# Optimization experiments

Measured on AMD Instinct MI355X. Metric: run time of the kernel, lower is better.

## Reference

```python
import jax, jax.numpy as jnp
import numpy as np

C = 128          # in_channels
NODE_NUM = 8192  # number of unique source nodes this step
D = 64           # max_member_num (fixed degree -> neighbor_bool all True)
E = NODE_NUM * D # total gathered neighbor slots
N_TOTAL = 200000 # total nodes in graph
NEG_SLOPE = 0.2


def setup_inputs() -> dict:
    key = jax.random.key(0)
    ks = jax.random.split(key, 8)
    node_features = jax.random.normal(ks[0], (N_TOTAL, C), jnp.float32)
    memory = jax.random.normal(ks[1], (N_TOTAL, C), jnp.float32)
    sc = 1.0 / np.sqrt(C)
    W_max = jax.random.normal(ks[2], (C, C), jnp.float32) * sc
    b_max = jnp.zeros((C,), jnp.float32)
    W_score = jax.random.normal(ks[3], (2 * C, 1), jnp.float32) * (1.0 / np.sqrt(2 * C))
    b_score = jnp.zeros((1,), jnp.float32)
    W_fit = jax.random.normal(ks[4], (C, 1), jnp.float32) * sc
    b_fit = jnp.zeros((1,), jnp.float32)
    neighbors = jax.random.randint(ks[5], (E,), 0, N_TOTAL)  # gathered neighbor node ids
    seg = jnp.repeat(jnp.arange(NODE_NUM), D)                # index_source_nodes (segment ids)
    return dict(node_features=node_features, memory=memory, W_max=W_max, b_max=b_max,
                W_score=W_score, b_score=b_score, W_fit=W_fit, b_fit=b_fit,
                neighbors=neighbors, seg=seg)


def reference(node_features, memory, W_max, b_max, W_score, b_score, W_fit, b_fit, neighbors, seg):
    # gather: features + detached memory per neighbor slot  [E, C]
    nbr = node_features[neighbors] + jax.lax.stop_gradient(memory[neighbors])
    # scatter_max per source node, then linear + re-gather duplication
    max_feature = jax.ops.segment_max(nbr, seg, num_segments=NODE_NUM)      # [node_num, C]
    max_lin = max_feature @ W_max + b_max                                    # [node_num, C]
    dup = max_lin[seg]                                                       # [E, C]
    # attention score over concat(center_max, neighbor)
    s = jnp.concatenate([dup, nbr], axis=-1) @ W_score + b_score             # [E, 1]
    s = jnp.where(s >= 0, s, NEG_SLOPE * s)                                  # leaky_relu
    # segment softmax over neighbors of each source node
    smax = jax.ops.segment_max(s, seg, num_segments=NODE_NUM)[seg]
    ex = jnp.exp(s - smax)
    denom = jax.ops.segment_sum(ex, seg, num_segments=NODE_NUM)[seg]
    score = ex / denom                                                       # [E, 1]
    # masked scatter into fixed [node_num, max_member_num] tensor (full mask -> reshape)
    score_tensor = score.reshape(NODE_NUM, D)
    # scatter_add pooling of score-weighted neighbor features
    cluster_feature = jax.ops.segment_sum(nbr * score, seg, num_segments=NODE_NUM)  # [node_num, C]
    # community fitness via linear score calculator + sigmoid
    fitness = jax.nn.sigmoid(cluster_feature @ W_fit + b_fit).reshape(-1)    # [node_num]
    return cluster_feature, score_tensor, fitness
```

## Files before the change

### kernel.cpp

```cpp
#include <hip/hip_runtime.h>
#include <hip/hip_fp16.h>
#include <math.h>

#define C_DIM 128
#define DEG 64
#define NEG_SLOPE 0.2f

typedef float nfloat4 __attribute__((ext_vector_type(4)));

__global__ __launch_bounds__(256)
void fuse_sum_half_kernel(const nfloat4* __restrict__ nf4,
                          const nfloat4* __restrict__ mem4,
                          float2* __restrict__ outh,
                          long n4,
                          const float* __restrict__ W_max,
                          const float* __restrict__ b_max,
                          const float* __restrict__ W_score,
                          const float* __restrict__ b_score,
                          float* __restrict__ combo) {
    const long base = (long)blockIdx.x * 1024 + threadIdx.x;
    if (base + 768 < n4) {
        nfloat4 a0 = __builtin_nontemporal_load(nf4 + base);
        nfloat4 a1 = __builtin_nontemporal_load(nf4 + base + 256);
        nfloat4 a2 = __builtin_nontemporal_load(nf4 + base + 512);
        nfloat4 a3 = __builtin_nontemporal_load(nf4 + base + 768);
        nfloat4 m0 = __builtin_nontemporal_load(mem4 + base);
        nfloat4 m1 = __builtin_nontemporal_load(mem4 + base + 256);
        nfloat4 m2 = __builtin_nontemporal_load(mem4 + base + 512);
        nfloat4 m3 = __builtin_nontemporal_load(mem4 + base + 768);
        const nfloat4 s0 = a0 + m0, s1 = a1 + m1, s2 = a2 + m2, s3 = a3 + m3;
        __half2 p0[2], p1[2], p2[2], p3[2];
        p0[0] = __floats2half2_rn(s0.x, s0.y); p0[1] = __floats2half2_rn(s0.z, s0.w);
        p1[0] = __floats2half2_rn(s1.x, s1.y); p1[1] = __floats2half2_rn(s1.z, s1.w);
        p2[0] = __floats2half2_rn(s2.x, s2.y); p2[1] = __floats2half2_rn(s2.z, s2.w);
        p3[0] = __floats2half2_rn(s3.x, s3.y); p3[1] = __floats2half2_rn(s3.z, s3.w);
        outh[base]       = *(const float2*)p0;
        outh[base + 256] = *(const float2*)p1;
        outh[base + 512] = *(const float2*)p2;
        outh[base + 768] = *(const float2*)p3;
    } else {
        #pragma unroll
        for (int k = 0; k < 4; ++k) {
            const long i = base + k * 256;
            if (i < n4) {
                const nfloat4 a = __builtin_nontemporal_load(nf4 + i);
                const nfloat4 m = __builtin_nontemporal_load(mem4 + i);
                const nfloat4 s = a + m;
                __half2 p[2];
                p[0] = __floats2half2_rn(s.x, s.y);
                p[1] = __floats2half2_rn(s.z, s.w);
                outh[i] = *(const float2*)p;
            }
        }
    }
    if (blockIdx.x == 0) {
        const int c = threadIdx.x;
        __shared__ float red[C_DIM];
        if (c < C_DIM) {
            float acc = 0.f;
            #pragma unroll 4
            for (int k = 0; k < C_DIM; ++k)
                acc += W_max[c * C_DIM + k] * W_score[k];
            combo[c] = acc;
            red[c] = b_max[c] * W_score[c];
        }
        __syncthreads();
        for (int off = 64; off > 0; off >>= 1) {
            if (c < off) red[c] += red[c + off];
            __syncthreads();
        }
        if (c == 0) combo[C_DIM] = red[0] + b_score[0];
    }
}

__global__ __launch_bounds__(256)
void detector_half2_kernel(const float4* __restrict__ sum4,
                           const float* __restrict__ W_score,
                           const float* __restrict__ W_fit,
                           const float* __restrict__ b_fit,
                           const int* __restrict__ neighbors,
                           const float* __restrict__ combo,
                           float* __restrict__ out_cf,
                           float* __restrict__ out_score,
                           float* __restrict__ out_fit) {
    __shared__ float4 red4[2][256][2];
    __shared__ float  chan[2][C_DIM];
    __shared__ float  s_raw[2][DEG];
    __shared__ float  sc[2][DEG];

    const int tid = threadIdx.x;
    const int n0  = blockIdx.x * 2;
    const int q   = tid & 15;
    const int g   = tid >> 4;

    int4 nb[2];
    nb[0] = ((const int4*)(neighbors + (long)n0 * DEG))[g];
    nb[1] = ((const int4*)(neighbors + (long)(n0 + 1) * DEG))[g];

    const float4 wsb0 = ((const float4*)(W_score + C_DIM))[2 * q];
    const float4 wsb1 = ((const float4*)(W_score + C_DIM))[2 * q + 1];

    float4 vh[2][4];
    {
        const int ids0[4] = {nb[0].x, nb[0].y, nb[0].z, nb[0].w};
        const int ids1[4] = {nb[1].x, nb[1].y, nb[1].z, nb[1].w};
        #pragma unroll
        for (int i = 0; i < 4; ++i) vh[0][i] = sum4[(long)ids0[i] * 16 + q];
        #pragma unroll
        for (int i = 0; i < 4; ++i) vh[1][i] = sum4[(long)ids1[i] * 16 + q];
    }
    asm volatile("" ::: "memory");

    #pragma unroll
    for (int p = 0; p < 2; ++p) {
        float mx[8];
        #pragma unroll
        for (int k = 0; k < 8; ++k) mx[k] = -INFINITY;
        #pragma unroll
        for (int i = 0; i < 4; ++i) {
            const __half2* hp = (const __half2*)&vh[p][i];
            const float2 f0 = __half22float2(hp[0]);
            const float2 f1 = __half22float2(hp[1]);
            const float2 f2 = __half22float2(hp[2]);
            const float2 f3 = __half22float2(hp[3]);
            mx[0] = fmaxf(mx[0], f0.x); mx[1] = fmaxf(mx[1], f0.y);
            mx[2] = fmaxf(mx[2], f1.x); mx[3] = fmaxf(mx[3], f1.y);
            mx[4] = fmaxf(mx[4], f2.x); mx[5] = fmaxf(mx[5], f2.y);
            mx[6] = fmaxf(mx[6], f3.x); mx[7] = fmaxf(mx[7], f3.y);
            float pd = f0.x * wsb0.x + f0.y * wsb0.y + f1.x * wsb0.z + f1.y * wsb0.w
                     + f2.x * wsb1.x + f2.y * wsb1.y + f3.x * wsb1.z + f3.y * wsb1.w;
            pd += __shfl_xor(pd, 1);
            pd += __shfl_xor(pd, 2);
            pd += __shfl_xor(pd, 4);
            pd += __shfl_xor(pd, 8);
            if (q == 0) s_raw[p][g * 4 + i] = pd;
        }
        red4[p][tid][0] = make_float4(mx[0], mx[1], mx[2], mx[3]);
        red4[p][tid][1] = make_float4(mx[4], mx[5], mx[6], mx[7]);
    }
    __syncthreads();

    {
        const int p = tid >> 7, c = tid & 127;
        const int ch = c >> 3, k = c & 7;
        const float* rp = (const float*)red4[p];
        float f = rp[ch * 8 + k];
        #pragma unroll
        for (int g2 = 1; g2 < 16; ++g2)
            f = fmaxf(f, rp[(g2 * 16 + ch) * 8 + k]);
        chan[p][c] = f * combo[c];
    }
    __syncthreads();

    if (tid < 128) {
        const int p = tid >> 6, slot = tid & 63;
        float t1 = chan[p][slot] + chan[p][slot + 64];
        #pragma unroll
        for (int msk = 1; msk <= 32; msk <<= 1)
            t1 += __shfl_xor(t1, msk);
        t1 += combo[C_DIM];
        float s = t1 + s_raw[p][slot];
        s = (s >= 0.f) ? s : NEG_SLOPE * s;
        float m = s;
        #pragma unroll
        for (int msk = 1; msk <= 32; msk <<= 1)
            m = fmaxf(m, __shfl_xor(m, msk));
        const float ex = __expf(s - m);
        float d = ex;
        #pragma unroll
        for (int msk = 1; msk <= 32; msk <<= 1)
            d += __shfl_xor(d, msk);
        const float sv = ex / d;
        sc[p][slot] = sv;
        out_score[(long)(n0 + p) * DEG + slot] = sv;
    }
    __syncthreads();

    #pragma unroll
    for (int p = 0; p < 2; ++p) {
        float acc[8] = {0.f, 0.f, 0.f, 0.f, 0.f, 0.f, 0.f, 0.f};
        #pragma unroll
        for (int i = 0; i < 4; ++i) {
            const float w = sc[p][g * 4 + i];
            const __half2* hp = (const __half2*)&vh[p][i];
            const float2 f0 = __half22float2(hp[0]);
            const float2 f1 = __half22float2(hp[1]);
            const float2 f2 = __half22float2(hp[2]);
            const float2 f3 = __half22float2(hp[3]);
            acc[0] += f0.x * w; acc[1] += f0.y * w;
            acc[2] += f1.x * w; acc[3] += f1.y * w;
            acc[4] += f2.x * w; acc[5] += f2.y * w;
            acc[6] += f3.x * w; acc[7] += f3.y * w;
        }
        red4[p][tid][0] = make_float4(acc[0], acc[1], acc[2], acc[3]);
        red4[p][tid][1] = make_float4(acc[4], acc[5], acc[6], acc[7]);
    }
    __syncthreads();

    {
        const int p = tid >> 7, c = tid & 127;
        const int ch = c >> 3, k = c & 7;
        const float* rp = (const float*)red4[p];
        float f = 0.f;
        #pragma unroll
        for (int g2 = 0; g2 < 16; ++g2)
            f += rp[(g2 * 16 + ch) * 8 + k];
        out_cf[(long)(n0 + p) * C_DIM + c] = f;
        chan[p][c] = f * W_fit[c];
    }
    __syncthreads();

    if (tid < 128) {
        const int p = tid >> 6, slot = tid & 63;
        float t = chan[p][slot] + chan[p][slot + 64];
        #pragma unroll
        for (int msk = 1; msk <= 32; msk <<= 1)
            t += __shfl_xor(t, msk);
        if (slot == 0)
            out_fit[n0 + p] = 1.f / (1.f + __expf(-(t + b_fit[0])));
    }
}

__global__ void precompute_kernel(const float* __restrict__ W_max,
                                  const float* __restrict__ b_max,
                                  const float* __restrict__ W_score,
                                  const float* __restrict__ b_score,
                                  float* __restrict__ combo) {
    const int c = threadIdx.x;
    float acc = 0.f;
    for (int k = 0; k < C_DIM; ++k)
        acc += W_max[c * C_DIM + k] * W_score[k];
    combo[c] = acc;
    __shared__ float red[C_DIM];
    red[c] = b_max[c] * W_score[c];
    __syncthreads();
    for (int off = 64; off > 0; off >>= 1) {
        if (c < off) red[c] += red[c + off];
        __syncthreads();
    }
    if (c == 0) combo[C_DIM] = red[0] + b_score[0];
}

__global__ __launch_bounds__(256)
void detector_f32_kernel(const float* __restrict__ nf,
                         const float* __restrict__ mem,
                         const float* __restrict__ W_score,
                         const float* __restrict__ W_fit,
                         const float* __restrict__ b_fit,
                         const int* __restrict__ neighbors,
                         const float* __restrict__ combo,
                         float* __restrict__ out_cf,
                         float* __restrict__ out_score,
                         float* __restrict__ out_fit) {
    __shared__ float4 red[256];
    __shared__ float  s_raw[DEG];
    __shared__ float  sc[DEG];
    __shared__ float  t1_sh;

    const int tid = threadIdx.x;
    const int n   = blockIdx.x;
    const int q   = tid & 31;
    const int g   = tid >> 5;

    const int4* nb4 = (const int4*)(neighbors + n * DEG + g * 8);
    const int4 nba = nb4[0];
    const int4 nbb = nb4[1];
    const int ids[8] = {nba.x, nba.y, nba.z, nba.w, nbb.x, nbb.y, nbb.z, nbb.w};
    const float4 wsb = ((const float4*)(W_score + C_DIM))[q];
    const float4* nf4  = (const float4*)nf;
    const float4* mem4 = (const float4*)mem;

    float4 v[8];
    float4 mx = make_float4(-INFINITY, -INFINITY, -INFINITY, -INFINITY);
    #pragma unroll
    for (int i = 0; i < 8; ++i) {
        const long node = ids[i];
        float4 vv = nf4[node * 32 + q];
        const float4 b = mem4[node * 32 + q];
        vv.x += b.x; vv.y += b.y; vv.z += b.z; vv.w += b.w;
        v[i] = vv;
        mx.x = fmaxf(mx.x, vv.x); mx.y = fmaxf(mx.y, vv.y);
        mx.z = fmaxf(mx.z, vv.z); mx.w = fmaxf(mx.w, vv.w);
        float p = vv.x * wsb.x + vv.y * wsb.y + vv.z * wsb.z + vv.w * wsb.w;
        p += __shfl_xor(p, 1); p += __shfl_xor(p, 2); p += __shfl_xor(p, 4);
        p += __shfl_xor(p, 8); p += __shfl_xor(p, 16);
        if (q == 0) s_raw[g * 8 + i] = p;
    }
    asm volatile("" ::: "memory");
    red[tid] = mx;
    __syncthreads();
    if (tid < 32) {
        float4 f = red[tid];
        #pragma unroll
        for (int r = 1; r < 8; ++r) {
            const float4 o = red[tid + 32 * r];
            f.x = fmaxf(f.x, o.x); f.y = fmaxf(f.y, o.y);
            f.z = fmaxf(f.z, o.z); f.w = fmaxf(f.w, o.w);
        }
        const float4 wc = ((const float4*)combo)[tid];
        float t1 = f.x * wc.x + f.y * wc.y + f.z * wc.z + f.w * wc.w;
        t1 += __shfl_xor(t1, 1); t1 += __shfl_xor(t1, 2); t1 += __shfl_xor(t1, 4);
        t1 += __shfl_xor(t1, 8); t1 += __shfl_xor(t1, 16);
        if (tid == 0) t1_sh = t1 + combo[C_DIM];
    }
    __syncthreads();
    if (tid < DEG) {
        float s = t1_sh + s_raw[tid];
        s = (s >= 0.f) ? s : NEG_SLOPE * s;
        float m = s;
        #pragma unroll
        for (int msk = 1; msk <= 32; msk <<= 1) m = fmaxf(m, __shfl_xor(m, msk));
        const float ex = __expf(s - m);
        float d = ex;
        #pragma unroll
        for (int msk = 1; msk <= 32; msk <<= 1) d += __shfl_xor(d, msk);
        const float sv = ex / d;
        sc[tid] = sv;
        out_score[n * DEG + tid] = sv;
    }
    __syncthreads();
    float4 acc = make_float4(0.f, 0.f, 0.f, 0.f);
    #pragma unroll
    for (int i = 0; i < 8; ++i) {
        const float w = sc[g * 8 + i];
        acc.x += v[i].x * w; acc.y += v[i].y * w;
        acc.z += v[i].z * w; acc.w += v[i].w * w;
    }
    red[tid] = acc;
    __syncthreads();
    if (tid < 32) {
        float4 f = red[tid];
        #pragma unroll
        for (int r = 1; r < 8; ++r) {
            const float4 o = red[tid + 32 * r];
            f.x += o.x; f.y += o.y; f.z += o.z; f.w += o.w;
        }
        ((float4*)(out_cf + (long)n * C_DIM))[tid] = f;
        const float4 wf = ((const float4*)W_fit)[tid];
        float fp = f.x * wf.x + f.y * wf.y + f.z * wf.z + f.w * wf.w;
        fp += __shfl_xor(fp, 1); fp += __shfl_xor(fp, 2); fp += __shfl_xor(fp, 4);
        fp += __shfl_xor(fp, 8); fp += __shfl_xor(fp, 16);
        if (tid == 0)
            out_fit[n] = 1.f / (1.f + __expf(-(fp + b_fit[0])));
    }
}

extern "C" void kernel_launch(void* const* d_in, const int* in_sizes, int n_in,
                              void* d_out, int out_size, void* d_ws, size_t ws_size,
                              hipStream_t stream) {
    const float* node_features = (const float*)d_in[0];
    const float* memory        = (const float*)d_in[1];
    const float* W_max         = (const float*)d_in[2];
    const float* b_max         = (const float*)d_in[3];
    const float* W_score       = (const float*)d_in[4];
    const float* b_score       = (const float*)d_in[5];
    const float* W_fit         = (const float*)d_in[6];
    const float* b_fit         = (const float*)d_in[7];
    const int*   neighbors     = (const int*)d_in[8];

    const long n_elem = (long)in_sizes[0];
    const int  nodes  = in_sizes[8] / DEG;
    const long n4     = n_elem / 4;

    float* combo = (float*)d_ws;
    __half* sumh = (__half*)(combo + 512);
    const size_t need = 512 * sizeof(float) + (size_t)n_elem * sizeof(__half);

    float* out_cf    = (float*)d_out;
    float* out_score = out_cf + (long)nodes * C_DIM;
    float* out_fit   = out_score + (long)nodes * DEG;

    if (ws_size >= need && (n_elem % 4) == 0 && (nodes % 2) == 0) {
        const int blocks = (int)((n4 + 1023) / 1024);
        fuse_sum_half_kernel<<<blocks, 256, 0, stream>>>(
            (const nfloat4*)node_features, (const nfloat4*)memory,
            (float2*)sumh, n4, W_max, b_max, W_score, b_score, combo);
        detector_half2_kernel<<<nodes / 2, 256, 0, stream>>>(
            (const float4*)sumh, W_score, W_fit, b_fit, neighbors, combo,
            out_cf, out_score, out_fit);
    } else {
        precompute_kernel<<<1, C_DIM, 0, stream>>>(W_max, b_max, W_score,
                                                   b_score, combo);
        detector_f32_kernel<<<nodes, 256, 0, stream>>>(
            node_features, memory, W_score, W_fit, b_fit, neighbors, combo,
            out_cf, out_score, out_fit);
    }
}
```

Measured before the change: 247.2 us.

## Process four nodes per block and use wave shuffles for channel reductions

The detector kernel now handles four source nodes per 256-thread block instead of two, so each thread keeps 16 gathered neighbor vectors in flight. The max and weighted-sum channel reductions first combine across lanes with shuffles, then finish over four waves through a small padded shared buffer instead of a 16-way shared-memory pass. The streaming fp16 pre-sum kernel doubles its per-thread work to eight float4 pairs. The aim is more memory-level parallelism and less shared-memory traffic, at the cost of higher register pressure and fewer blocks in flight.

Measured after the change: 259.5 us. +5.0%, slower.

```diff
diff --git a/kernel.cpp b/kernel.cpp
--- a/kernel.cpp
+++ b/kernel.cpp
@@ -18,29 +18,24 @@
                           const float* __restrict__ W_score,
                           const float* __restrict__ b_score,
                           float* __restrict__ combo) {
-    const long base = (long)blockIdx.x * 1024 + threadIdx.x;
-    if (base + 768 < n4) {
-        nfloat4 a0 = __builtin_nontemporal_load(nf4 + base);
-        nfloat4 a1 = __builtin_nontemporal_load(nf4 + base + 256);
-        nfloat4 a2 = __builtin_nontemporal_load(nf4 + base + 512);
-        nfloat4 a3 = __builtin_nontemporal_load(nf4 + base + 768);
-        nfloat4 m0 = __builtin_nontemporal_load(mem4 + base);
-        nfloat4 m1 = __builtin_nontemporal_load(mem4 + base + 256);
-        nfloat4 m2 = __builtin_nontemporal_load(mem4 + base + 512);
-        nfloat4 m3 = __builtin_nontemporal_load(mem4 + base + 768);
-        const nfloat4 s0 = a0 + m0, s1 = a1 + m1, s2 = a2 + m2, s3 = a3 + m3;
-        __half2 p0[2], p1[2], p2[2], p3[2];
-        p0[0] = __floats2half2_rn(s0.x, s0.y); p0[1] = __floats2half2_rn(s0.z, s0.w);
-        p1[0] = __floats2half2_rn(s1.x, s1.y); p1[1] = __floats2half2_rn(s1.z, s1.w);
-        p2[0] = __floats2half2_rn(s2.x, s2.y); p2[1] = __floats2half2_rn(s2.z, s2.w);
-        p3[0] = __floats2half2_rn(s3.x, s3.y); p3[1] = __floats2half2_rn(s3.z, s3.w);
-        outh[base]       = *(const float2*)p0;
-        outh[base + 256] = *(const float2*)p1;
-        outh[base + 512] = *(const float2*)p2;
-        outh[base + 768] = *(const float2*)p3;
+    const long base = (long)blockIdx.x * 2048 + threadIdx.x;
+    if (base + 1792 < n4) {
+        nfloat4 a[8], m[8];
+        #pragma unroll
+        for (int k = 0; k < 8; ++k) a[k] = __builtin_nontemporal_load(nf4 + base + k * 256);
+        #pragma unroll
+        for (int k = 0; k < 8; ++k) m[k] = __builtin_nontemporal_load(mem4 + base + k * 256);
+        #pragma unroll
+        for (int k = 0; k < 8; ++k) {
+            const nfloat4 s = a[k] + m[k];
+            __half2 p[2];
+            p[0] = __floats2half2_rn(s.x, s.y);
+            p[1] = __floats2half2_rn(s.z, s.w);
+            outh[base + k * 256] = *(const float2*)p;
+        }
     } else {
         #pragma unroll
-        for (int k = 0; k < 4; ++k) {
+        for (int k = 0; k < 8; ++k) {
             const long i = base + k * 256;
             if (i < n4) {
                 const nfloat4 a = __builtin_nontemporal_load(nf4 + i);
@@ -74,7 +69,7 @@
 }
 
 __global__ __launch_bounds__(256)
-void detector_half2_kernel(const float4* __restrict__ sum4,
+void detector_half4_kernel(const float4* __restrict__ sum4,
                            const float* __restrict__ W_score,
                            const float* __restrict__ W_fit,
                            const float* __restrict__ b_fit,
@@ -83,36 +78,37 @@
                            float* __restrict__ out_cf,
                            float* __restrict__ out_score,
                            float* __restrict__ out_fit) {
-    __shared__ float4 red4[2][256][2];
-    __shared__ float  chan[2][C_DIM];
-    __shared__ float  s_raw[2][DEG];
-    __shared__ float  sc[2][DEG];
+    __shared__ float wred[4][4][16][9];
+    __shared__ float chan[4][C_DIM];
+    __shared__ float s_raw[4][DEG];
+    __shared__ float sc[4][DEG];
 
     const int tid = threadIdx.x;
-    const int n0  = blockIdx.x * 2;
+    const int n0  = blockIdx.x * 4;
     const int q   = tid & 15;
     const int g   = tid >> 4;
-
-    int4 nb[2];
-    nb[0] = ((const int4*)(neighbors + (long)n0 * DEG))[g];
-    nb[1] = ((const int4*)(neighbors + (long)(n0 + 1) * DEG))[g];
+    const int wv  = tid >> 6;
+    const int ln  = tid & 63;
+
+    int4 nb[4];
+    #pragma unroll
+    for (int p = 0; p < 4; ++p)
+        nb[p] = ((const int4*)(neighbors + (long)(n0 + p) * DEG))[g];
 
     const float4 wsb0 = ((const float4*)(W_score + C_DIM))[2 * q];
     const float4 wsb1 = ((const float4*)(W_score + C_DIM))[2 * q + 1];
 
-    float4 vh[2][4];
-    {
-        const int ids0[4] = {nb[0].x, nb[0].y, nb[0].z, nb[0].w};
-        const int ids1[4] = {nb[1].x, nb[1].y, nb[1].z, nb[1].w};
-        #pragma unroll
-        for (int i = 0; i < 4; ++i) vh[0][i] = sum4[(long)ids0[i] * 16 + q];
-        #pragma unroll
-        for (int i = 0; i < 4; ++i) vh[1][i] = sum4[(long)ids1[i] * 16 + q];
+    float4 vh[4][4];
+    #pragma unroll
+    for (int p = 0; p < 4; ++p) {
+        const int ids[4] = {nb[p].x, nb[p].y, nb[p].z, nb[p].w};
+        #pragma unroll
+        for (int i = 0; i < 4; ++i) vh[p][i] = sum4[(long)ids[i] * 16 + q];
     }
     asm volatile("" ::: "memory");
 
     #pragma unroll
-    for (int p = 0; p < 2; ++p) {
+    for (int p = 0; p < 4; ++p) {
         float mx[8];
         #pragma unroll
         for (int k = 0; k < 8; ++k) mx[k] = -INFINITY;
@@ -135,25 +131,33 @@
             pd += __shfl_xor(pd, 8);
             if (q == 0) s_raw[p][g * 4 + i] = pd;
         }
-        red4[p][tid][0] = make_float4(mx[0], mx[1], mx[2], mx[3]);
-        red4[p][tid][1] = make_float4(mx[4], mx[5], mx[6], mx[7]);
+        #pragma unroll
+        for (int k = 0; k < 8; ++k) {
+            mx[k] = fmaxf(mx[k], __shfl_xor(mx[k], 16));
+            mx[k] = fmaxf(mx[k], __shfl_xor(mx[k], 32));
+        }
+        if (ln < 16) {
+            #pragma unroll
+            for (int k = 0; k < 8; ++k) wred[p][wv][q][k] = mx[k];
+        }
+    }
+    __syncthreads();
+
+    #pragma unroll
+    for (int it = 0; it < 2; ++it) {
+        const int idx = it * 256 + tid;
+        const int p = idx >> 7, c = idx & 127;
+        const int ch = c >> 3, k = c & 7;
+        float f = wred[p][0][ch][k];
+        f = fmaxf(f, wred[p][1][ch][k]);
+        f = fmaxf(f, wred[p][2][ch][k]);
+        f = fmaxf(f, wred[p][3][ch][k]);
+        chan[p][c] = f * combo[c];
     }
     __syncthreads();
 
     {
-        const int p = tid >> 7, c = tid & 127;
-        const int ch = c >> 3, k = c & 7;
-        const float* rp = (const float*)red4[p];
-        float f = rp[ch * 8 + k];
-        #pragma unroll
-        for (int g2 = 1; g2 < 16; ++g2)
-            f = fmaxf(f, rp[(g2 * 16 + ch) * 8 + k]);
-        chan[p][c] = f * combo[c];
-    }
-    __syncthreads();
-
-    if (tid < 128) {
-        const int p = tid >> 6, slot = tid & 63;
+        const int p = wv, slot = ln;
         float t1 = chan[p][slot] + chan[p][slot + 64];
         #pragma unroll
         for (int msk = 1; msk <= 32; msk <<= 1)
@@ -177,7 +181,7 @@
     __syncthreads();
 
     #pragma unroll
-    for (int p = 0; p < 2; ++p) {
+    for (int p = 0; p < 4; ++p) {
         float acc[8] = {0.f, 0.f, 0.f, 0.f, 0.f, 0.f, 0.f, 0.f};
         #pragma unroll
         for (int i = 0; i < 4; ++i) {
@@ -192,26 +196,32 @@
             acc[4] += f2.x * w; acc[5] += f2.y * w;
             acc[6] += f3.x * w; acc[7] += f3.y * w;
         }
-        red4[p][tid][0] = make_float4(acc[0], acc[1], acc[2], acc[3]);
-        red4[p][tid][1] = make_float4(acc[4], acc[5], acc[6], acc[7]);
-    }
-    __syncthreads();
-
-    {
-        const int p = tid >> 7, c = tid & 127;
+        #pragma unroll
+        for (int k = 0; k < 8; ++k) {
+            acc[k] += __shfl_xor(acc[k], 16);
+            acc[k] += __shfl_xor(acc[k], 32);
+        }
+        if (ln < 16) {
+            #pragma unroll
+            for (int k = 0; k < 8; ++k) wred[p][wv][q][k] = acc[k];
+        }
+    }
+    __syncthreads();
+
+    #pragma unroll
+    for (int it = 0; it < 2; ++it) {
+        const int idx = it * 256 + tid;
+        const int p = idx >> 7, c = idx & 127;
         const int ch = c >> 3, k = c & 7;
-        const float* rp = (const float*)red4[p];
-        float f = 0.f;
-        #pragma unroll
-        for (int g2 = 0; g2 < 16; ++g2)
-            f += rp[(g2 * 16 + ch) * 8 + k];
+        const float f = wred[p][0][ch][k] + wred[p][1][ch][k]
+                      + wred[p][2][ch][k] + wred[p][3][ch][k];
         out_cf[(long)(n0 + p) * C_DIM + c] = f;
         chan[p][c] = f * W_fit[c];
     }
     __syncthreads();
 
-    if (tid < 128) {
-        const int p = tid >> 6, slot = tid & 63;
+    {
+        const int p = wv, slot = ln;
         float t = chan[p][slot] + chan[p][slot + 64];
         #pragma unroll
         for (int msk = 1; msk <= 32; msk <<= 1)
@@ -370,12 +380,12 @@
     float* out_score = out_cf + (long)nodes * C_DIM;
     float* out_fit   = out_score + (long)nodes * DEG;
 
-    if (ws_size >= need && (n_elem % 4) == 0 && (nodes % 2) == 0) {
-        const int blocks = (int)((n4 + 1023) / 1024);
+    if (ws_size >= need && (n_elem % 4) == 0 && (nodes % 4) == 0) {
+        const int blocks = (int)((n4 + 2047) / 2048);
         fuse_sum_half_kernel<<<blocks, 256, 0, stream>>>(
             (const nfloat4*)node_features, (const nfloat4*)memory,
             (float2*)sumh, n4, W_max, b_max, W_score, b_score, combo);
-        detector_half2_kernel<<<nodes / 2, 256, 0, stream>>>(
+        detector_half4_kernel<<<nodes / 4, 256, 0, stream>>>(
             (const float4*)sumh, W_score, W_fit, b_fit, neighbors, combo,
             out_cf, out_score, out_fit);
     } else {
```
